# Kernel optimization log

Hardware: AMD Instinct MI355X
Metric: run time of the kernel (lower is better)

Reference implementation:

```python
import jax, jax.numpy as jnp
import numpy as np

IN_FEAT = 512
D_FEAT = 512
N_HEAD = 8
EPS = 1e-5
NEG = -1e9


def setup_inputs() -> dict:
    key = jax.random.key(0)
    ks = jax.random.split(key, 12)
    B, C, T = 8, IN_FEAT, 2048
    s_in = 1.0 / np.sqrt(IN_FEAT)
    s_d = 1.0 / np.sqrt(D_FEAT)
    return {
        "x": jax.random.normal(ks[0], (B, C, T), dtype=jnp.float32),
        "gamma": jnp.ones((IN_FEAT,), dtype=jnp.float32),
        "beta": jnp.zeros((IN_FEAT,), dtype=jnp.float32),
        "wq": jax.random.uniform(ks[1], (IN_FEAT, D_FEAT), jnp.float32, -s_in, s_in),
        "bq": jax.random.uniform(ks[2], (D_FEAT,), jnp.float32, -s_in, s_in),
        "wk": jax.random.uniform(ks[3], (IN_FEAT, D_FEAT), jnp.float32, -s_in, s_in),
        "bk": jax.random.uniform(ks[4], (D_FEAT,), jnp.float32, -s_in, s_in),
        "wv": jax.random.uniform(ks[5], (IN_FEAT, D_FEAT), jnp.float32, -s_in, s_in),
        "bv": jax.random.uniform(ks[6], (D_FEAT,), jnp.float32, -s_in, s_in),
        "wo": jax.random.uniform(ks[7], (D_FEAT, IN_FEAT), jnp.float32, -s_d, s_d),
        "bo": jax.random.uniform(ks[8], (IN_FEAT,), jnp.float32, -s_d, s_d),
    }


def reference(x, gamma, beta, wq, bq, wk, bk, wv, bv, wo, bo):
    # x: (B, Cin, T)
    resi = x
    h = jnp.swapaxes(x, -2, -1)  # (B, T, Cin)
    mu = jnp.mean(h, axis=-1, keepdims=True)
    var = jnp.mean(jnp.square(h - mu), axis=-1, keepdims=True)
    h = (h - mu) / jnp.sqrt(var + EPS) * gamma + beta

    B, T, _ = h.shape
    dh = D_FEAT // N_HEAD
    scale = np.sqrt(dh).astype(np.float32)

    def split_heads(y):  # (B,T,D) -> (B,H,T,dh)
        return jnp.swapaxes(y.reshape(B, T, N_HEAD, dh), 1, 2)

    q = split_heads(h @ wq + bq)
    k = split_heads(h @ wk + bk)
    v = split_heads(h @ wv + bv)

    scores = jnp.einsum('bhqd,bhkd->bhqk', q, k) / scale  # (B,H,T,T)
    mask = jnp.triu(jnp.ones((T, T), dtype=scores.dtype), k=1)  # strict upper
    scores = scores + NEG * mask
    attn = jax.nn.softmax(scores, axis=-1)
    ctx = jnp.einsum('bhqk,bhkd->bhqd', attn, v)  # (B,H,T,dh)
    ctx = jnp.swapaxes(ctx, 1, 2).reshape(B, T, D_FEAT)
    out = jnp.swapaxes(ctx @ wo + bo, -2, -1)  # (B, Cin, T)
    return resi + out
```

## Files before the change

### kernel.cpp

```cpp
#include <hip/hip_runtime.h>
#include <hip/hip_bf16.h>

#define BB 8
#define TT 2048
#define CC 512
#define DD 512
#define HH 8
#define DH 64

typedef __bf16 bf16x8 __attribute__((ext_vector_type(8)));
typedef __bf16 bf16x4 __attribute__((ext_vector_type(4)));
typedef float  f32x4  __attribute__((ext_vector_type(4)));

static __device__ __forceinline__ bf16x8 concat4(bf16x4 a, bf16x4 b) {
    bf16x8 r;
    #pragma unroll
    for (int i = 0; i < 4; ++i) { r[i] = a[i]; r[i + 4] = b[i]; }
    return r;
}

__global__ __launch_bounds__(256) void ln_kernel(
    const float* __restrict__ x, const float* __restrict__ gamma,
    const float* __restrict__ beta, __hip_bfloat16* __restrict__ h)
{
    const int b  = blockIdx.x >> 6;
    const int t0 = (blockIdx.x & 63) * 32;
    const int tid = threadIdx.x;
    const int tl = tid & 31;
    const int part = tid >> 5;

    const float* xb = x + (size_t)b * CC * TT;

    float sum = 0.f, sq = 0.f;
    for (int ci = 0; ci < 64; ++ci) {
        int c = part * 64 + ci;
        float v = xb[(size_t)c * TT + t0 + tl];
        sum += v; sq += v * v;
    }
    __shared__ float sA[8][32], sB[8][32];
    sA[part][tl] = sum; sB[part][tl] = sq;
    __syncthreads();
    __shared__ float s_mu[32], s_rstd[32];
    if (part == 0) {
        float s = 0.f, q = 0.f;
        for (int p = 0; p < 8; ++p) { s += sA[p][tl]; q += sB[p][tl]; }
        float mu  = s * (1.0f / 512.0f);
        float var = q * (1.0f / 512.0f) - mu * mu;
        s_mu[tl] = mu;
        s_rstd[tl] = rsqrtf(var + 1e-5f);
    }
    __syncthreads();

    const float mu = s_mu[tl], rstd = s_rstd[tl];
    __shared__ __hip_bfloat16 tileT[32][72];

    for (int chunk = 0; chunk < 8; ++chunk) {
        int cb = chunk * 64 + part * 8;
        #pragma unroll
        for (int j = 0; j < 8; ++j) {
            int c = cb + j;
            float v = xb[(size_t)c * TT + t0 + tl];
            float nv = (v - mu) * rstd * gamma[c] + beta[c];
            tileT[tl][part * 8 + j] = __float2bfloat16(nv);
        }
        __syncthreads();
        int cl = tid & 63, tw = tid >> 6;
        #pragma unroll
        for (int k = 0; k < 8; ++k) {
            int t = tw + k * 4;
            h[((size_t)(b * TT + t0 + t)) * CC + chunk * 64 + cl] = tileT[t][cl];
        }
        __syncthreads();
    }
}

__global__ __launch_bounds__(256) void prepack_w4(
    const float* __restrict__ w0, const float* __restrict__ w1,
    const float* __restrict__ w2, const float* __restrict__ w3,
    __hip_bfloat16* __restrict__ o0, __hip_bfloat16* __restrict__ o1,
    __hip_bfloat16* __restrict__ o2, __hip_bfloat16* __restrict__ o3)
{
    const float* w; __hip_bfloat16* wt;
    switch (blockIdx.y) {
        case 0: w = w0; wt = o0; break;
        case 1: w = w1; wt = o1; break;
        case 2: w = w2; wt = o2; break;
        default: w = w3; wt = o3; break;
    }
    __shared__ float tile[32][33];
    const int bx = blockIdx.x & 15;
    const int by = blockIdx.x >> 4;
    const int lx = threadIdx.x & 31, ly = threadIdx.x >> 5;
    #pragma unroll
    for (int i = 0; i < 4; ++i) {
        int k = by * 32 + ly + i * 8;
        tile[ly + i * 8][lx] = w[(size_t)k * 512 + bx * 32 + lx];
    }
    __syncthreads();
    #pragma unroll
    for (int i = 0; i < 4; ++i) {
        int n = bx * 32 + ly + i * 8;
        wt[(size_t)n * 512 + by * 32 + lx] = __float2bfloat16(tile[lx][ly + i * 8]);
    }
}

__global__ __launch_bounds__(256) void qkv_gemm(
    const __hip_bfloat16* __restrict__ A,
    const __hip_bfloat16* __restrict__ wtq, const __hip_bfloat16* __restrict__ wtk,
    const __hip_bfloat16* __restrict__ wtv,
    const float* __restrict__ bq, const float* __restrict__ bk,
    const float* __restrict__ bv,
    __hip_bfloat16* __restrict__ qo, __hip_bfloat16* __restrict__ ko,
    __hip_bfloat16* __restrict__ vt)
{
    const int m0 = blockIdx.x * 128;
    const int n0 = blockIdx.y * 128;
    const __hip_bfloat16* WT; const float* bias; __hip_bfloat16* out;
    if (blockIdx.z == 0)      { WT = wtq; bias = bq; out = qo; }
    else if (blockIdx.z == 1) { WT = wtk; bias = bk; out = ko; }
    else                      { WT = wtv; bias = bv; out = vt; }
    const float sc = (blockIdx.z == 0) ? 0.18033688011112042f : 1.0f;

    __shared__ __hip_bfloat16 As[2][128][40];
    __shared__ __hip_bfloat16 Bs[2][128][40];
    __shared__ float eps[4][16][17];

    const int tid = threadIdx.x;
    const int wave = tid >> 6, lane = tid & 63;
    const int quad = lane >> 4, l16 = lane & 15;
    const int wy = wave >> 1, wx = wave & 1;

    const int srow = tid >> 2;
    const int skof = (tid & 3) * 8;

    f32x4 acc[4][4] = {};
    bf16x8 areg[2], breg[2];

    #pragma unroll
    for (int i = 0; i < 2; ++i) {
        int r = srow + i * 64;
        areg[i] = *reinterpret_cast<const bf16x8*>(&A[(size_t)(m0 + r) * 512 + skof]);
        breg[i] = *reinterpret_cast<const bf16x8*>(&WT[(size_t)(n0 + r) * 512 + skof]);
    }
    #pragma unroll
    for (int i = 0; i < 2; ++i) {
        int r = srow + i * 64;
        *reinterpret_cast<bf16x8*>(&As[0][r][skof]) = areg[i];
        *reinterpret_cast<bf16x8*>(&Bs[0][r][skof]) = breg[i];
    }
    __syncthreads();

    for (int kt = 0; kt < 512; kt += 32) {
        const int cur = (kt >> 5) & 1;
        const bool havenext = (kt + 32 < 512);
        if (havenext) {
            #pragma unroll
            for (int i = 0; i < 2; ++i) {
                int r = srow + i * 64;
                areg[i] = *reinterpret_cast<const bf16x8*>(
                    &A[(size_t)(m0 + r) * 512 + kt + 32 + skof]);
                breg[i] = *reinterpret_cast<const bf16x8*>(
                    &WT[(size_t)(n0 + r) * 512 + kt + 32 + skof]);
            }
        }
        bf16x8 af[4], bfr[4];
        #pragma unroll
        for (int mt = 0; mt < 4; ++mt)
            af[mt] = *reinterpret_cast<const bf16x8*>(&As[cur][wy * 64 + mt * 16 + l16][quad * 8]);
        #pragma unroll
        for (int nt = 0; nt < 4; ++nt)
            bfr[nt] = *reinterpret_cast<const bf16x8*>(&Bs[cur][wx * 64 + nt * 16 + l16][quad * 8]);
        #pragma unroll
        for (int mt = 0; mt < 4; ++mt)
            #pragma unroll
            for (int nt = 0; nt < 4; ++nt)
                acc[mt][nt] = __builtin_amdgcn_mfma_f32_16x16x32_bf16(
                    af[mt], bfr[nt], acc[mt][nt], 0, 0, 0);
        if (havenext) {
            #pragma unroll
            for (int i = 0; i < 2; ++i) {
                int r = srow + i * 64;
                *reinterpret_cast<bf16x8*>(&As[cur ^ 1][r][skof]) = areg[i];
                *reinterpret_cast<bf16x8*>(&Bs[cur ^ 1][r][skof]) = breg[i];
            }
        }
        __syncthreads();
    }

    if (blockIdx.z != 2) {
        #pragma unroll
        for (int nt = 0; nt < 4; ++nt) {
            int n = n0 + wx * 64 + nt * 16 + l16;
            int hh = n >> 6, di = n & 63;
            float bval = bias[n];
            #pragma unroll
            for (int mt = 0; mt < 4; ++mt) {
                #pragma unroll
                for (int r = 0; r < 4; ++r) {
                    int m = m0 + wy * 64 + mt * 16 + quad * 4 + r;
                    int b = m >> 11, t = m & 2047;
                    out[((size_t)((b * HH + hh) * TT + t)) * DH + di] =
                        __float2bfloat16((acc[mt][nt][r] + bval) * sc);
                }
            }
        }
    } else {
        #pragma unroll
        for (int mt = 0; mt < 4; ++mt) {
            int mbase = m0 + wy * 64 + mt * 16;
            #pragma unroll
            for (int nt = 0; nt < 4; ++nt) {
                int ncol = n0 + wx * 64 + nt * 16 + l16;
                float bval = bias[ncol];
                #pragma unroll
                for (int r = 0; r < 4; ++r)
                    eps[wave][quad * 4 + r][l16] = acc[mt][nt][r] + bval;
                #pragma unroll
                for (int pass = 0; pass < 4; ++pass) {
                    int nl = pass * 4 + quad;
                    int n = n0 + wx * 64 + nt * 16 + nl;
                    int hh = n >> 6, di = n & 63;
                    int m = mbase + l16;
                    int b = m >> 11, t = m & 2047;
                    out[((size_t)((b * HH + hh) * DH + di)) * TT + t] =
                        __float2bfloat16(eps[wave][l16][nl]);
                }
            }
        }
    }
}

static __device__ __forceinline__ void attn_tile(
    const __hip_bfloat16 (*Ksb)[72], const __hip_bfloat16 (*Vtsb)[72],
    int k0, int q0, int wave, int quad, int l16,
    const bf16x8 (&qf)[2][2], f32x4 (&o_acc)[4][2], float (&l_run)[2])
{
    f32x4 s[2][4];
    #pragma unroll
    for (int nt = 0; nt < 4; ++nt) {
        bf16x8 kf0 = *reinterpret_cast<const bf16x8*>(&Ksb[nt * 16 + l16][quad * 8]);
        bf16x8 kf1 = *reinterpret_cast<const bf16x8*>(&Ksb[nt * 16 + l16][32 + quad * 8]);
        #pragma unroll
        for (int mt = 0; mt < 2; ++mt) {
            f32x4 z = {};
            z = __builtin_amdgcn_mfma_f32_16x16x32_bf16(kf0, qf[mt][0], z, 0, 0, 0);
            z = __builtin_amdgcn_mfma_f32_16x16x32_bf16(kf1, qf[mt][1], z, 0, 0, 0);
            s[mt][nt] = z;
        }
    }
    bf16x4 pt[2][4];
    #pragma unroll
    for (int mt = 0; mt < 2; ++mt) {
        const int qrow = q0 + wave * 32 + mt * 16 + l16;
        const bool fullun = (k0 + 63 <= q0 + wave * 32 + mt * 16);
        float lsum = 0.f;
        #pragma unroll
        for (int nt = 0; nt < 4; ++nt) {
            #pragma unroll
            for (int r = 0; r < 4; ++r) {
                float p = __builtin_amdgcn_exp2f(s[mt][nt][r]);
                if (!fullun) {
                    int key = k0 + nt * 16 + quad * 4 + r;
                    if (key > qrow) p = 0.f;
                }
                lsum += p;
                pt[mt][nt][r] = (__bf16)p;
            }
        }
        l_run[mt] += lsum;
    }
    #pragma unroll
    for (int cp = 0; cp < 2; ++cp) {
        bf16x8 pfr[2];
        #pragma unroll
        for (int mt = 0; mt < 2; ++mt)
            pfr[mt] = concat4(pt[mt][cp * 2], pt[mt][cp * 2 + 1]);
        #pragma unroll
        for (int dt = 0; dt < 4; ++dt) {
            bf16x4 va = *reinterpret_cast<const bf16x4*>(
                &Vtsb[dt * 16 + l16][cp * 32 + quad * 4]);
            bf16x4 vb = *reinterpret_cast<const bf16x4*>(
                &Vtsb[dt * 16 + l16][cp * 32 + 16 + quad * 4]);
            bf16x8 vf = concat4(va, vb);
            #pragma unroll
            for (int mt = 0; mt < 2; ++mt)
                o_acc[dt][mt] = __builtin_amdgcn_mfma_f32_16x16x32_bf16(
                    vf, pfr[mt], o_acc[dt][mt], 0, 0, 0);
        }
    }
}

__global__ __launch_bounds__(256, 2) void attn_kernel(
    const __hip_bfloat16* __restrict__ Q, const __hip_bfloat16* __restrict__ K,
    const __hip_bfloat16* __restrict__ Vt, __hip_bfloat16* __restrict__ ctx)
{
    const int xi = blockIdx.x;
    const int bh = blockIdx.y;
    const int q0h = (15 - xi) * 128;
    const int q0l = xi * 128;
    const __hip_bfloat16* Qb  = Q  + (size_t)bh * TT * DH;
    const __hip_bfloat16* Kb  = K  + (size_t)bh * TT * DH;
    const __hip_bfloat16* Vtb = Vt + (size_t)bh * DH * TT;

    const int tid = threadIdx.x, wave = tid >> 6, lane = tid & 63;
    const int quad = lane >> 4, l16 = lane & 15;

    __shared__ __hip_bfloat16 Ks[2][64][72];
    __shared__ __hip_bfloat16 Vts[2][64][72];

    bf16x8 qfh[2][2], qfl[2][2];
    #pragma unroll
    for (int mt = 0; mt < 2; ++mt) {
        int rh = q0h + wave * 32 + mt * 16 + l16;
        int rl = q0l + wave * 32 + mt * 16 + l16;
        #pragma unroll
        for (int st = 0; st < 2; ++st) {
            qfh[mt][st] = *reinterpret_cast<const bf16x8*>(
                &Qb[(size_t)rh * DH + st * 32 + quad * 8]);
            qfl[mt][st] = *reinterpret_cast<const bf16x8*>(
                &Qb[(size_t)rl * DH + st * 32 + quad * 8]);
        }
    }

    f32x4 oh[4][2] = {}, ol[4][2] = {};
    float lh[2] = {0.f, 0.f}, ll[2] = {0.f, 0.f};

    const int rr = tid >> 3;
    const int co = (tid & 7) * 8;

    bf16x8 kreg[2], vreg[2];
    #pragma unroll
    for (int i = 0; i < 2; ++i) {
        int r2 = rr + i * 32;
        kreg[i] = *reinterpret_cast<const bf16x8*>(&Kb[(size_t)r2 * DH + co]);
        vreg[i] = *reinterpret_cast<const bf16x8*>(&Vtb[(size_t)r2 * TT + co]);
    }
    #pragma unroll
    for (int i = 0; i < 2; ++i) {
        int r2 = rr + i * 32;
        *reinterpret_cast<bf16x8*>(&Ks[0][r2][co]) = kreg[i];
        *reinterpret_cast<bf16x8*>(&Vts[0][r2][co]) = vreg[i];
    }
    __syncthreads();

    const int nsteps = q0h / 64 + 2;
    for (int step = 0; step < nsteps; ++step) {
        const int k0 = step * 64;
        const int cur = step & 1;
        const bool havenext = (step + 1 < nsteps);
        if (havenext) {
            const int kn = k0 + 64;
            #pragma unroll
            for (int i = 0; i < 2; ++i) {
                int r2 = rr + i * 32;
                kreg[i] = *reinterpret_cast<const bf16x8*>(
                    &Kb[(size_t)(kn + r2) * DH + co]);
                vreg[i] = *reinterpret_cast<const bf16x8*>(
                    &Vtb[(size_t)r2 * TT + kn + co]);
            }
        }
        if (k0 <= q0h + wave * 32 + 31)
            attn_tile(Ks[cur], Vts[cur], k0, q0h, wave, quad, l16, qfh, oh, lh);
        if (k0 <= q0l + wave * 32 + 31)
            attn_tile(Ks[cur], Vts[cur], k0, q0l, wave, quad, l16, qfl, ol, ll);
        if (havenext) {
            const int nxt = cur ^ 1;
            #pragma unroll
            for (int i = 0; i < 2; ++i) {
                int r2 = rr + i * 32;
                *reinterpret_cast<bf16x8*>(&Ks[nxt][r2][co]) = kreg[i];
                *reinterpret_cast<bf16x8*>(&Vts[nxt][r2][co]) = vreg[i];
            }
        }
        __syncthreads();
    }

    float invh[2], invl[2];
    #pragma unroll
    for (int mt = 0; mt < 2; ++mt) {
        float a = lh[mt];
        a += __shfl_xor(a, 16, 64); a += __shfl_xor(a, 32, 64);
        invh[mt] = 1.0f / a;
        float c = ll[mt];
        c += __shfl_xor(c, 16, 64); c += __shfl_xor(c, 32, 64);
        invl[mt] = 1.0f / c;
    }

    const int b = bh >> 3, hh = bh & 7;
    #pragma unroll
    for (int mt = 0; mt < 2; ++mt) {
        int th = q0h + wave * 32 + mt * 16 + l16;
        int tl2 = q0l + wave * 32 + mt * 16 + l16;
        #pragma unroll
        for (int dt = 0; dt < 4; ++dt) {
            bf16x4 pa, pb;
            #pragma unroll
            for (int r = 0; r < 4; ++r) {
                pa[r] = (__bf16)(oh[dt][mt][r] * invh[mt]);
                pb[r] = (__bf16)(ol[dt][mt][r] * invl[mt]);
            }
            *reinterpret_cast<bf16x4*>(
                &ctx[((size_t)(b * TT + th)) * DD + hh * DH + dt * 16 + quad * 4]) = pa;
            *reinterpret_cast<bf16x4*>(
                &ctx[((size_t)(b * TT + tl2)) * DD + hh * DH + dt * 16 + quad * 4]) = pb;
        }
    }
}

__global__ __launch_bounds__(256) void oproj_gemm(
    const __hip_bfloat16* __restrict__ WT, const __hip_bfloat16* __restrict__ Actx,
    const float* __restrict__ bo, const float* __restrict__ xres,
    float* __restrict__ outp)
{
    const int m0 = blockIdx.x * 128;
    const int n0 = blockIdx.y * 128;

    __shared__ __hip_bfloat16 As[2][128][40];
    __shared__ __hip_bfloat16 Bs[2][128][40];

    const int tid = threadIdx.x;
    const int wave = tid >> 6, lane = tid & 63;
    const int quad = lane >> 4, l16 = lane & 15;
    const int wy = wave >> 1, wx = wave & 1;

    const int srow = tid >> 2;
    const int skof = (tid & 3) * 8;

    f32x4 acc[4][4] = {};
    bf16x8 areg[2], breg[2];

    #pragma unroll
    for (int i = 0; i < 2; ++i) {
        int r = srow + i * 64;
        areg[i] = *reinterpret_cast<const bf16x8*>(&WT[(size_t)(m0 + r) * 512 + skof]);
        breg[i] = *reinterpret_cast<const bf16x8*>(&Actx[(size_t)(n0 + r) * 512 + skof]);
    }
    #pragma unroll
    for (int i = 0; i < 2; ++i) {
        int r = srow + i * 64;
        *reinterpret_cast<bf16x8*>(&As[0][r][skof]) = areg[i];
        *reinterpret_cast<bf16x8*>(&Bs[0][r][skof]) = breg[i];
    }
    __syncthreads();

    for (int kt = 0; kt < 512; kt += 32) {
        const int cur = (kt >> 5) & 1;
        const bool havenext = (kt + 32 < 512);
        if (havenext) {
            #pragma unroll
            for (int i = 0; i < 2; ++i) {
                int r = srow + i * 64;
                areg[i] = *reinterpret_cast<const bf16x8*>(
                    &WT[(size_t)(m0 + r) * 512 + kt + 32 + skof]);
                breg[i] = *reinterpret_cast<const bf16x8*>(
                    &Actx[(size_t)(n0 + r) * 512 + kt + 32 + skof]);
            }
        }
        bf16x8 af[4], bfr[4];
        #pragma unroll
        for (int mt = 0; mt < 4; ++mt)
            af[mt] = *reinterpret_cast<const bf16x8*>(&As[cur][wy * 64 + mt * 16 + l16][quad * 8]);
        #pragma unroll
        for (int nt = 0; nt < 4; ++nt)
            bfr[nt] = *reinterpret_cast<const bf16x8*>(&Bs[cur][wx * 64 + nt * 16 + l16][quad * 8]);
        #pragma unroll
        for (int mt = 0; mt < 4; ++mt)
            #pragma unroll
            for (int nt = 0; nt < 4; ++nt)
                acc[mt][nt] = __builtin_amdgcn_mfma_f32_16x16x32_bf16(
                    af[mt], bfr[nt], acc[mt][nt], 0, 0, 0);
        if (havenext) {
            #pragma unroll
            for (int i = 0; i < 2; ++i) {
                int r = srow + i * 64;
                *reinterpret_cast<bf16x8*>(&As[cur ^ 1][r][skof]) = areg[i];
                *reinterpret_cast<bf16x8*>(&Bs[cur ^ 1][r][skof]) = breg[i];
            }
        }
        __syncthreads();
    }

    #pragma unroll
    for (int mt = 0; mt < 4; ++mt) {
        #pragma unroll
        for (int nt = 0; nt < 4; ++nt) {
            int tg = n0 + wx * 64 + nt * 16 + l16;
            int b = tg >> 11, t = tg & 2047;
            #pragma unroll
            for (int r = 0; r < 4; ++r) {
                int c = m0 + wy * 64 + mt * 16 + quad * 4 + r;
                size_t oi = ((size_t)(b * CC + c)) * TT + t;
                outp[oi] = xres[oi] + acc[mt][nt][r] + bo[c];
            }
        }
    }
}

extern "C" void kernel_launch(void* const* d_in, const int* in_sizes, int n_in,
                              void* d_out, int out_size, void* d_ws, size_t ws_size,
                              hipStream_t stream)
{
    const float* x     = (const float*)d_in[0];
    const float* gamma = (const float*)d_in[1];
    const float* beta  = (const float*)d_in[2];
    const float* wq    = (const float*)d_in[3];
    const float* bq    = (const float*)d_in[4];
    const float* wk    = (const float*)d_in[5];
    const float* bk    = (const float*)d_in[6];
    const float* wv    = (const float*)d_in[7];
    const float* bv    = (const float*)d_in[8];
    const float* wo    = (const float*)d_in[9];
    const float* bo    = (const float*)d_in[10];
    float* out = (float*)d_out;

    char* ws = (char*)d_ws;
    const size_t sz_big = (size_t)BB * TT * DD * sizeof(__hip_bfloat16);
    __hip_bfloat16* hbf = (__hip_bfloat16*)ws; ws += sz_big;
    __hip_bfloat16* qb  = (__hip_bfloat16*)ws; ws += sz_big;
    __hip_bfloat16* kb  = (__hip_bfloat16*)ws; ws += sz_big;
    __hip_bfloat16* vtb = (__hip_bfloat16*)ws; ws += sz_big;
    __hip_bfloat16* ctx = (__hip_bfloat16*)ws; ws += sz_big;
    const size_t sz_w = (size_t)512 * 512 * sizeof(__hip_bfloat16);
    __hip_bfloat16* wtq = (__hip_bfloat16*)ws; ws += sz_w;
    __hip_bfloat16* wtk = (__hip_bfloat16*)ws; ws += sz_w;
    __hip_bfloat16* wtv = (__hip_bfloat16*)ws; ws += sz_w;
    __hip_bfloat16* wto = (__hip_bfloat16*)ws; ws += sz_w;

    prepack_w4<<<dim3(256, 4), 256, 0, stream>>>(wq, wk, wv, wo,
                                                 wtq, wtk, wtv, wto);

    ln_kernel<<<BB * (TT / 32), 256, 0, stream>>>(x, gamma, beta, hbf);

    qkv_gemm<<<dim3(BB * TT / 128, DD / 128, 3), 256, 0, stream>>>(
        hbf, wtq, wtk, wtv, bq, bk, bv, qb, kb, vtb);

    attn_kernel<<<dim3(8, BB * HH), 256, 0, stream>>>(qb, kb, vtb, ctx);

    oproj_gemm<<<dim3(CC / 128, BB * TT / 128), 256, 0, stream>>>(
        wto, ctx, bo, x, out);
}
```

Baseline: 241.7 us.

## Use async global-to-LDS loads with XOR swizzle in GEMMs; cache x in LN

Both GEMM kernels drop the register-staged double-buffered loads and load 64-wide K tiles directly into an XOR-swizzled LDS layout with global_load_lds. This is meant to cut VGPR traffic, halve the barrier count and avoid bank conflicts. The V projection swaps the MFMA operands so the transposed output can be written directly, dropping the shared-memory transpose buffer. The LayerNorm kernel keeps x in a 64KB LDS tile so it is not read from global memory twice. The GEMMs now run single-buffered, with no overlap between load and compute, and the larger LDS use in the LayerNorm kernel may lower its occupancy.

```diff
diff --git a/kernel.cpp b/kernel.cpp
--- a/kernel.cpp
+++ b/kernel.cpp
@@ -19,6 +19,12 @@
     return r;
 }
 
+static __device__ __forceinline__ void async_ld16(const void* g, void* l) {
+    __builtin_amdgcn_global_load_lds(
+        (const __attribute__((address_space(1))) void*)g,
+        (__attribute__((address_space(3))) void*)l, 16, 0, 0);
+}
+
 __global__ __launch_bounds__(256) void ln_kernel(
     const float* __restrict__ x, const float* __restrict__ gamma,
     const float* __restrict__ beta, __hip_bfloat16* __restrict__ h)
@@ -31,10 +37,13 @@
 
     const float* xb = x + (size_t)b * CC * TT;
 
+    __shared__ float xs[512][32];
     float sum = 0.f, sq = 0.f;
+    #pragma unroll 8
     for (int ci = 0; ci < 64; ++ci) {
         int c = part * 64 + ci;
         float v = xb[(size_t)c * TT + t0 + tl];
+        xs[c][tl] = v;
         sum += v; sq += v * v;
     }
     __shared__ float sA[8][32], sB[8][32];
@@ -59,8 +68,7 @@
         #pragma unroll
         for (int j = 0; j < 8; ++j) {
             int c = cb + j;
-            float v = xb[(size_t)c * TT + t0 + tl];
-            float nv = (v - mu) * rstd * gamma[c] + beta[c];
+            float nv = (xs[c][tl] - mu) * rstd * gamma[c] + beta[c];
             tileT[tl][part * 8 + j] = __float2bfloat16(nv);
         }
         __syncthreads();
@@ -120,74 +128,63 @@
     else if (blockIdx.z == 1) { WT = wtk; bias = bk; out = ko; }
     else                      { WT = wtv; bias = bv; out = vt; }
     const float sc = (blockIdx.z == 0) ? 0.18033688011112042f : 1.0f;
-
-    __shared__ __hip_bfloat16 As[2][128][40];
-    __shared__ __hip_bfloat16 Bs[2][128][40];
-    __shared__ float eps[4][16][17];
+    const bool vswap = (blockIdx.z == 2);
+
+    __shared__ __hip_bfloat16 As[128][64];
+    __shared__ __hip_bfloat16 Bs[128][64];
 
     const int tid = threadIdx.x;
     const int wave = tid >> 6, lane = tid & 63;
     const int quad = lane >> 4, l16 = lane & 15;
     const int wy = wave >> 1, wx = wave & 1;
 
-    const int srow = tid >> 2;
-    const int skof = (tid & 3) * 8;
+    const int r8 = lane >> 3;
+    const int c8 = lane & 7;
+    const int cg = (c8 ^ r8) * 8;
 
     f32x4 acc[4][4] = {};
-    bf16x8 areg[2], breg[2];
-
-    #pragma unroll
-    for (int i = 0; i < 2; ++i) {
-        int r = srow + i * 64;
-        areg[i] = *reinterpret_cast<const bf16x8*>(&A[(size_t)(m0 + r) * 512 + skof]);
-        breg[i] = *reinterpret_cast<const bf16x8*>(&WT[(size_t)(n0 + r) * 512 + skof]);
-    }
-    #pragma unroll
-    for (int i = 0; i < 2; ++i) {
-        int r = srow + i * 64;
-        *reinterpret_cast<bf16x8*>(&As[0][r][skof]) = areg[i];
-        *reinterpret_cast<bf16x8*>(&Bs[0][r][skof]) = breg[i];
-    }
-    __syncthreads();
-
-    for (int kt = 0; kt < 512; kt += 32) {
-        const int cur = (kt >> 5) & 1;
-        const bool havenext = (kt + 32 < 512);
-        if (havenext) {
-            #pragma unroll
-            for (int i = 0; i < 2; ++i) {
-                int r = srow + i * 64;
-                areg[i] = *reinterpret_cast<const bf16x8*>(
-                    &A[(size_t)(m0 + r) * 512 + kt + 32 + skof]);
-                breg[i] = *reinterpret_cast<const bf16x8*>(
-                    &WT[(size_t)(n0 + r) * 512 + kt + 32 + skof]);
-            }
-        }
-        bf16x8 af[4], bfr[4];
-        #pragma unroll
-        for (int mt = 0; mt < 4; ++mt)
-            af[mt] = *reinterpret_cast<const bf16x8*>(&As[cur][wy * 64 + mt * 16 + l16][quad * 8]);
-        #pragma unroll
-        for (int nt = 0; nt < 4; ++nt)
-            bfr[nt] = *reinterpret_cast<const bf16x8*>(&Bs[cur][wx * 64 + nt * 16 + l16][quad * 8]);
-        #pragma unroll
-        for (int mt = 0; mt < 4; ++mt)
+
+    for (int kt = 0; kt < 512; kt += 64) {
+        #pragma unroll
+        for (int i = 0; i < 4; ++i) {
+            int rbase = wave * 32 + i * 8;
+            int row = rbase + r8;
+            async_ld16(&A[(size_t)(m0 + row) * 512 + kt + cg], &As[rbase][0]);
+            async_ld16(&WT[(size_t)(n0 + row) * 512 + kt + cg], &Bs[rbase][0]);
+        }
+        __syncthreads();
+        #pragma unroll
+        for (int kk = 0; kk < 2; ++kk) {
+            const int xr = l16 & 7;
+            bf16x8 af[4], bfr[4];
+            #pragma unroll
+            for (int mt = 0; mt < 4; ++mt)
+                af[mt] = *reinterpret_cast<const bf16x8*>(
+                    &As[wy * 64 + mt * 16 + l16][((kk * 4 + quad) ^ xr) * 8]);
             #pragma unroll
             for (int nt = 0; nt < 4; ++nt)
-                acc[mt][nt] = __builtin_amdgcn_mfma_f32_16x16x32_bf16(
-                    af[mt], bfr[nt], acc[mt][nt], 0, 0, 0);
-        if (havenext) {
-            #pragma unroll
-            for (int i = 0; i < 2; ++i) {
-                int r = srow + i * 64;
-                *reinterpret_cast<bf16x8*>(&As[cur ^ 1][r][skof]) = areg[i];
-                *reinterpret_cast<bf16x8*>(&Bs[cur ^ 1][r][skof]) = breg[i];
-            }
-        }
-        __syncthreads();
-    }
-
-    if (blockIdx.z != 2) {
+                bfr[nt] = *reinterpret_cast<const bf16x8*>(
+                    &Bs[wx * 64 + nt * 16 + l16][((kk * 4 + quad) ^ xr) * 8]);
+            if (!vswap) {
+                #pragma unroll
+                for (int mt = 0; mt < 4; ++mt)
+                    #pragma unroll
+                    for (int nt = 0; nt < 4; ++nt)
+                        acc[mt][nt] = __builtin_amdgcn_mfma_f32_16x16x32_bf16(
+                            af[mt], bfr[nt], acc[mt][nt], 0, 0, 0);
+            } else {
+                #pragma unroll
+                for (int mt = 0; mt < 4; ++mt)
+                    #pragma unroll
+                    for (int nt = 0; nt < 4; ++nt)
+                        acc[mt][nt] = __builtin_amdgcn_mfma_f32_16x16x32_bf16(
+                            bfr[nt], af[mt], acc[mt][nt], 0, 0, 0);
+            }
+        }
+        __syncthreads();
+    }
+
+    if (!vswap) {
         #pragma unroll
         for (int nt = 0; nt < 4; ++nt) {
             int n = n0 + wx * 64 + nt * 16 + l16;
@@ -206,24 +203,18 @@
         }
     } else {
         #pragma unroll
-        for (int mt = 0; mt < 4; ++mt) {
-            int mbase = m0 + wy * 64 + mt * 16;
-            #pragma unroll
-            for (int nt = 0; nt < 4; ++nt) {
-                int ncol = n0 + wx * 64 + nt * 16 + l16;
-                float bval = bias[ncol];
+        for (int nt = 0; nt < 4; ++nt) {
+            #pragma unroll
+            for (int r = 0; r < 4; ++r) {
+                int n = n0 + wx * 64 + nt * 16 + quad * 4 + r;
+                int hh = n >> 6, di = n & 63;
+                float bval = bias[n];
                 #pragma unroll
-                for (int r = 0; r < 4; ++r)
-                    eps[wave][quad * 4 + r][l16] = acc[mt][nt][r] + bval;
-                #pragma unroll
-                for (int pass = 0; pass < 4; ++pass) {
-                    int nl = pass * 4 + quad;
-                    int n = n0 + wx * 64 + nt * 16 + nl;
-                    int hh = n >> 6, di = n & 63;
-                    int m = mbase + l16;
+                for (int mt = 0; mt < 4; ++mt) {
+                    int m = m0 + wy * 64 + mt * 16 + l16;
                     int b = m >> 11, t = m & 2047;
                     out[((size_t)((b * HH + hh) * DH + di)) * TT + t] =
-                        __float2bfloat16(eps[wave][l16][nl]);
+                        __float2bfloat16(acc[mt][nt][r] + bval);
                 }
             }
         }
@@ -415,67 +406,47 @@
     const int m0 = blockIdx.x * 128;
     const int n0 = blockIdx.y * 128;
 
-    __shared__ __hip_bfloat16 As[2][128][40];
-    __shared__ __hip_bfloat16 Bs[2][128][40];
+    __shared__ __hip_bfloat16 As[128][64];
+    __shared__ __hip_bfloat16 Bs[128][64];
 
     const int tid = threadIdx.x;
     const int wave = tid >> 6, lane = tid & 63;
     const int quad = lane >> 4, l16 = lane & 15;
     const int wy = wave >> 1, wx = wave & 1;
 
-    const int srow = tid >> 2;
-    const int skof = (tid & 3) * 8;
+    const int r8 = lane >> 3;
+    const int c8 = lane & 7;
+    const int cg = (c8 ^ r8) * 8;
 
     f32x4 acc[4][4] = {};
-    bf16x8 areg[2], breg[2];
-
-    #pragma unroll
-    for (int i = 0; i < 2; ++i) {
-        int r = srow + i * 64;
-        areg[i] = *reinterpret_cast<const bf16x8*>(&WT[(size_t)(m0 + r) * 512 + skof]);
-        breg[i] = *reinterpret_cast<const bf16x8*>(&Actx[(size_t)(n0 + r) * 512 + skof]);
-    }
-    #pragma unroll
-    for (int i = 0; i < 2; ++i) {
-        int r = srow + i * 64;
-        *reinterpret_cast<bf16x8*>(&As[0][r][skof]) = areg[i];
-        *reinterpret_cast<bf16x8*>(&Bs[0][r][skof]) = breg[i];
-    }
-    __syncthreads();
-
-    for (int kt = 0; kt < 512; kt += 32) {
-        const int cur = (kt >> 5) & 1;
-        const bool havenext = (kt + 32 < 512);
-        if (havenext) {
-            #pragma unroll
-            for (int i = 0; i < 2; ++i) {
-                int r = srow + i * 64;
-                areg[i] = *reinterpret_cast<const bf16x8*>(
-                    &WT[(size_t)(m0 + r) * 512 + kt + 32 + skof]);
-                breg[i] = *reinterpret_cast<const bf16x8*>(
-                    &Actx[(size_t)(n0 + r) * 512 + kt + 32 + skof]);
-            }
-        }
-        bf16x8 af[4], bfr[4];
-        #pragma unroll
-        for (int mt = 0; mt < 4; ++mt)
-            af[mt] = *reinterpret_cast<const bf16x8*>(&As[cur][wy * 64 + mt * 16 + l16][quad * 8]);
-        #pragma unroll
-        for (int nt = 0; nt < 4; ++nt)
-            bfr[nt] = *reinterpret_cast<const bf16x8*>(&Bs[cur][wx * 64 + nt * 16 + l16][quad * 8]);
-        #pragma unroll
-        for (int mt = 0; mt < 4; ++mt)
+
+    for (int kt = 0; kt < 512; kt += 64) {
+        #pragma unroll
+        for (int i = 0; i < 4; ++i) {
+            int rbase = wave * 32 + i * 8;
+            int row = rbase + r8;
+            async_ld16(&WT[(size_t)(m0 + row) * 512 + kt + cg], &As[rbase][0]);
+            async_ld16(&Actx[(size_t)(n0 + row) * 512 + kt + cg], &Bs[rbase][0]);
+        }
+        __syncthreads();
+        #pragma unroll
+        for (int kk = 0; kk < 2; ++kk) {
+            const int xr = l16 & 7;
+            bf16x8 af[4], bfr[4];
+            #pragma unroll
+            for (int mt = 0; mt < 4; ++mt)
+                af[mt] = *reinterpret_cast<const bf16x8*>(
+                    &As[wy * 64 + mt * 16 + l16][((kk * 4 + quad) ^ xr) * 8]);
             #pragma unroll
             for (int nt = 0; nt < 4; ++nt)
-                acc[mt][nt] = __builtin_amdgcn_mfma_f32_16x16x32_bf16(
-                    af[mt], bfr[nt], acc[mt][nt], 0, 0, 0);
-        if (havenext) {
-            #pragma unroll
-            for (int i = 0; i < 2; ++i) {
-                int r = srow + i * 64;
-                *reinterpret_cast<bf16x8*>(&As[cur ^ 1][r][skof]) = areg[i];
-                *reinterpret_cast<bf16x8*>(&Bs[cur ^ 1][r][skof]) = breg[i];
-            }
+                bfr[nt] = *reinterpret_cast<const bf16x8*>(
+                    &Bs[wx * 64 + nt * 16 + l16][((kk * 4 + quad) ^ xr) * 8]);
+            #pragma unroll
+            for (int mt = 0; mt < 4; ++mt)
+                #pragma unroll
+                for (int nt = 0; nt < 4; ++nt)
+                    acc[mt][nt] = __builtin_amdgcn_mfma_f32_16x16x32_bf16(
+                        af[mt], bfr[nt], acc[mt][nt], 0, 0, 0);
         }
         __syncthreads();
     }
```

After: 224.0 us. 1.08x faster.
